# Kernel optimization log

Measured on AMD Instinct MI355X. Metric: run time of the kernel, lower is better.

The kernel has to match this reference:

```python
import jax, jax.numpy as jnp
import numpy as np

B, S, D, H = 2, 2048, 2048, 16
DH = D // H
NEG = -1000000000.0


def setup_inputs() -> dict:
    key = jax.random.key(0)
    ks = jax.random.split(key, 5)
    return {
        "query_vector": jax.random.normal(ks[0], (B, S, D), dtype=jnp.float32),
        "key_vector": jax.random.normal(ks[1], (B, S, D), dtype=jnp.float32),
        "value_vector": jax.random.normal(ks[2], (B, S, D), dtype=jnp.float32),
        "W_qkv": jax.random.normal(ks[3], (D, 3 * D), dtype=jnp.float32) * (1.0 / np.sqrt(D)),
        "b_qkv": jax.random.normal(ks[4], (3 * D,), dtype=jnp.float32) * 0.01,
    }


def reference(query_vector, key_vector, value_vector, W_qkv, b_qkv):
    # NOTE: original forward only consumes query_vector; key/value args unused.
    qkv = query_vector @ W_qkv + b_qkv                      # [B, S, 3D]
    q, k, v = jnp.split(qkv, 3, axis=-1)                    # each [B, S, D]
    # Faithful to original: plain reshape (NOT transpose) into heads.
    q = q.reshape(B, H, S, DH)
    k = k.reshape(B, H, S, DH)
    v = v.reshape(B, H, S, DH)
    scores = jnp.einsum("bhqd,bhkd->bhqk", q, k) / np.float32(np.sqrt(DH))
    # torch.triu_indices(offset=0): mask j >= i (diagonal included), SET to -1e9.
    idx = jnp.arange(S)
    causal = idx[None, :] >= idx[:, None]                   # [S, S], True where masked
    scores = jnp.where(causal, jnp.float32(NEG), scores)
    attn = jax.nn.softmax(scores, axis=-1)
    out = jnp.einsum("bhqk,bhkd->bhqd", attn, v)            # [B, H, S, DH]
    # dropout is identity in eval mode
    return out.reshape(B, S, D)
```

## Files before the change

kernel.cpp:

```cpp
#include <hip/hip_runtime.h>
#include <hip/hip_bf16.h>
#include <stdint.h>

typedef unsigned short u16;
typedef short short8 __attribute__((ext_vector_type(8)));
typedef short short4v __attribute__((ext_vector_type(4)));
typedef float f32x4 __attribute__((ext_vector_type(4)));

#define CSL (0.08838834764831845f * 1.4426950408889634f)
#define NEGR -1.0e13f


__device__ __forceinline__ u16 f2b(float f) {
  union { float f; unsigned int u; } c; c.f = f;
  unsigned int u = c.u;
  u += 0x7fffu + ((u >> 16) & 1u);
  return (u16)(u >> 16);
}
__device__ __forceinline__ float b2f(u16 h) {
  union { float f; unsigned int u; } c; c.u = ((unsigned int)h) << 16;
  return c.f;
}

__global__ __launch_bounds__(256) void k_cast_q(const float* __restrict__ in, u16* __restrict__ out) {
  size_t idx = ((size_t)blockIdx.x * 256 + threadIdx.x) * 8;
  float4 f0 = *(const float4*)(in + idx);
  float4 f1 = *(const float4*)(in + idx + 4);
  short8 o;
  o[0] = (short)f2b(f0.x); o[1] = (short)f2b(f0.y); o[2] = (short)f2b(f0.z); o[3] = (short)f2b(f0.w);
  o[4] = (short)f2b(f1.x); o[5] = (short)f2b(f1.y); o[6] = (short)f2b(f1.z); o[7] = (short)f2b(f1.w);
  *(short8*)(out + idx) = o;
}

__global__ __launch_bounds__(256) void k_cast_wt(const float* __restrict__ W, u16* __restrict__ Wt) {
  __shared__ u16 L[64 * 68];
  const int t = threadIdx.x;
  const int nb = blockIdx.x * 64;
  const int kb = blockIdx.y * 64;
#pragma unroll
  for (int it = 0; it < 4; ++it) {
    int idx = it * 1024 + t * 4;
    int r = idx >> 6, c = idx & 63;
    float4 f = *(const float4*)(W + (size_t)(kb + r) * 6144 + nb + c);
    L[r * 68 + c + 0] = f2b(f.x);
    L[r * 68 + c + 1] = f2b(f.y);
    L[r * 68 + c + 2] = f2b(f.z);
    L[r * 68 + c + 3] = f2b(f.w);
  }
  __syncthreads();
#pragma unroll
  for (int it = 0; it < 4; ++it) {
    int idx = it * 1024 + t * 4;
    int i = idx >> 6, j = idx & 63;
    short4v o;
#pragma unroll
    for (int e = 0; e < 4; ++e) o[e] = (short)L[(j + e) * 68 + i];
    *(short4v*)(Wt + (size_t)(nb + i) * 2048 + kb + j) = o;
  }
}

__global__ __launch_bounds__(256) void k_gemm(const u16* __restrict__ A,
                                              const u16* __restrict__ Bt,
                                              const float* __restrict__ bias,
                                              u16* __restrict__ qb,
                                              u16* __restrict__ kbuf,
                                              u16* __restrict__ vbuf) {
  __shared__ u16 As[128 * 32];
  __shared__ u16 Bs[128 * 32];
  const int t = threadIdx.x;
  const int ln = t & 63, wv = t >> 6;
  const int lr = ln & 15, lg = ln >> 4;
  const int mb = blockIdx.y * 128, nb = blockIdx.x * 128;
  const int wm = (wv >> 1) * 64, wn = (wv & 1) * 64;
  f32x4 acc[4][4] = {};
  for (int kt = 0; kt < 64; ++kt) {
    const int k0 = kt * 32;
#pragma unroll
    for (int it = 0; it < 2; ++it) {
      int chunk = it * 256 + wv * 64 + ln;
      int r = chunk >> 2, c8 = (chunk & 3) * 8;
      __builtin_amdgcn_global_load_lds(
          (const __attribute__((address_space(1))) void*)(A + (size_t)(mb + r) * 2048 + k0 + c8),
          (__attribute__((address_space(3))) void*)(As + (size_t)(it * 256 + wv * 64) * 8),
          16, 0, 0);
      __builtin_amdgcn_global_load_lds(
          (const __attribute__((address_space(1))) void*)(Bt + (size_t)(nb + r) * 2048 + k0 + c8),
          (__attribute__((address_space(3))) void*)(Bs + (size_t)(it * 256 + wv * 64) * 8),
          16, 0, 0);
    }
    __syncthreads();
    short8 af[4], bf[4];
#pragma unroll
    for (int mi = 0; mi < 4; ++mi)
      af[mi] = *(const short8*)(As + (wm + mi * 16 + lr) * 32 + lg * 8);
#pragma unroll
    for (int ni = 0; ni < 4; ++ni)
      bf[ni] = *(const short8*)(Bs + (wn + ni * 16 + lr) * 32 + lg * 8);
#pragma unroll
    for (int mi = 0; mi < 4; ++mi)
#pragma unroll
      for (int ni = 0; ni < 4; ++ni)
        acc[mi][ni] = __builtin_amdgcn_mfma_f32_16x16x32_bf16(af[mi], bf[ni], acc[mi][ni], 0, 0, 0);
    __syncthreads();
  }
  u16* dst = (nb < 2048) ? qb : (nb < 4096 ? kbuf : vbuf);
  const int nnb = nb & 2047;
#pragma unroll
  for (int ni = 0; ni < 4; ++ni) {
    int n = wn + ni * 16 + lr;
    float bv = bias[nb + n];
#pragma unroll
    for (int mi = 0; mi < 4; ++mi) {
#pragma unroll
      for (int r = 0; r < 4; ++r) {
        int m = mb + wm + mi * 16 + lg * 4 + r;
        dst[(size_t)m * 2048 + nnb + n] = f2b(acc[mi][ni][r] + bv);
      }
    }
  }
}

__global__ __launch_bounds__(256) void k_vtrans(const u16* __restrict__ v, u16* __restrict__ vt,
                                                float* __restrict__ part) {
  __shared__ u16 L[128 * 136];
  __shared__ float Ls2[256];
  const int t = threadIdx.x;
  const int bh = blockIdx.y, sc = blockIdx.x;
  const size_t base = (size_t)bh * 262144;
#pragma unroll
  for (int it = 0; it < 8; ++it) {
    int chunk = it * 256 + t;
    int s = chunk >> 4, d8 = (chunk & 15) * 8;
    *(short8*)(L + s * 136 + d8) = *(const short8*)(v + base + (size_t)(sc * 128 + s) * 128 + d8);
  }
  __syncthreads();
#pragma unroll
  for (int it = 0; it < 8; ++it) {
    int chunk = it * 256 + t;
    int dh = chunk >> 4, s8 = (chunk & 15) * 8;
    short8 o;
#pragma unroll
    for (int e = 0; e < 8; ++e) o[e] = (short)L[(s8 + e) * 136 + dh];
    *(short8*)(vt + base + (size_t)dh * 2048 + sc * 128 + s8) = o;
  }
  {
    const int dh = t & 127, seg = t >> 7;
    float ps = 0.f;
#pragma unroll 8
    for (int i = 0; i < 64; ++i) ps += b2f(L[(seg * 64 + i) * 136 + dh]);
    Ls2[t] = ps;
    __syncthreads();
    if (t < 128) part[((size_t)bh * 16 + sc) * 128 + t] = Ls2[t] + Ls2[t + 128];
  }
}

__global__ __launch_bounds__(256, 3) void k_attn(const u16* __restrict__ qb,
                                                 const u16* __restrict__ kb,
                                                 const u16* __restrict__ vt,
                                                 const float* __restrict__ part,
                                                 float* __restrict__ out) {
  __shared__ u16 Ks[64 * 136];
  __shared__ u16 Vs[128 * 72];
  __shared__ u16 Ps[4][16 * 72];
  const int t = threadIdx.x;
  const int ln = t & 63, wv = t >> 6;
  const int lr = ln & 15, lg = ln >> 4;
  const int L = blockIdx.y * 32 + blockIdx.x;
  const int wl = (L & 7) * 128 + (L >> 3);
  const int bh = wl >> 5;
  const int qt = 31 - (wl & 31);
  const size_t base = (size_t)bh * 262144;
  const u16* Qh = qb + base;
  const u16* Kh = kb + base;
  const u16* Vth = vt + base;
  float* Oh = out + base;
  const int qs = qt * 64;

  short8 qf[4];
  {
    int qr = qs + wv * 16 + lr;
#pragma unroll
    for (int ks = 0; ks < 4; ++ks)
      qf[ks] = *(const short8*)(Qh + (size_t)qr * 128 + ks * 32 + lg * 8);
  }
  float lsum[4] = {0.f, 0.f, 0.f, 0.f};
  f32x4 acc[8];
  const f32x4 fz = {0.f, 0.f, 0.f, 0.f};
#pragma unroll
  for (int oj = 0; oj < 8; ++oj) acc[oj] = fz;

  u16* Pw = &Ps[wv][0];
  const int nkt = qt + 1;
  for (int kt = 0; kt < nkt; ++kt) {
#pragma unroll
    for (int it = 0; it < 4; ++it) {
      int chunk = it * 256 + t;
      int sk = chunk >> 4, d8 = (chunk & 15) * 8;
      *(short8*)(Ks + sk * 136 + d8) = *(const short8*)(Kh + (size_t)(kt * 64 + sk) * 128 + d8);
    }
#pragma unroll
    for (int it = 0; it < 4; ++it) {
      int chunk = it * 256 + t;
      int dh = chunk >> 3, s8 = (chunk & 7) * 8;
      *(short8*)(Vs + dh * 72 + s8) = *(const short8*)(Vth + (size_t)dh * 2048 + kt * 64 + s8);
    }
    __syncthreads();

    f32x4 s[4];
#pragma unroll
    for (int ni = 0; ni < 4; ++ni) s[ni] = fz;
#pragma unroll
    for (int ks = 0; ks < 4; ++ks) {
#pragma unroll
      for (int ni = 0; ni < 4; ++ni) {
        short8 kf = *(const short8*)(Ks + (ni * 16 + lr) * 136 + ks * 32 + lg * 8);
        s[ni] = __builtin_amdgcn_mfma_f32_16x16x32_bf16(qf[ks], kf, s[ni], 0, 0, 0);
      }
    }
    if (kt == qt) {
#pragma unroll
      for (int ni = 0; ni < 4; ++ni) {
        int col = kt * 64 + ni * 16 + lr;
#pragma unroll
        for (int r = 0; r < 4; ++r) {
          int row = qs + wv * 16 + lg * 4 + r;
          if (col >= row) s[ni][r] = NEGR;
        }
      }
    }
#pragma unroll
    for (int ni = 0; ni < 4; ++ni)
#pragma unroll
      for (int r = 0; r < 4; ++r) {
        u16 h = f2b(exp2f(s[ni][r] * CSL));
        Pw[(lg * 4 + r) * 72 + ni * 16 + lr] = h;
        lsum[r] += b2f(h);
      }
#pragma unroll
    for (int ks2 = 0; ks2 < 2; ++ks2) {
      short8 pa = *(const short8*)(Pw + lr * 72 + ks2 * 32 + lg * 8);
#pragma unroll
      for (int oj = 0; oj < 8; ++oj) {
        short8 vf = *(const short8*)(Vs + (oj * 16 + lr) * 72 + ks2 * 32 + lg * 8);
        acc[oj] = __builtin_amdgcn_mfma_f32_16x16x32_bf16(pa, vf, acc[oj], 0, 0, 0);
      }
    }
    __syncthreads();
  }

  float rl[4];
#pragma unroll
  for (int r = 0; r < 4; ++r) {
    float sa = lsum[r];
#pragma unroll
    for (int d = 1; d < 16; d <<= 1) sa += __shfl_xor(sa, d, 64);
    rl[r] = 1.0f / sa;
  }
#pragma unroll
  for (int oj = 0; oj < 8; ++oj)
#pragma unroll
    for (int r = 0; r < 4; ++r) {
      int row = qs + wv * 16 + lg * 4 + r;
      float val = acc[oj][r] * rl[r];
      if (qt == 0 && wv == 0 && lg == 0 && r == 0) {
        float vs = 0.f;
#pragma unroll
        for (int sc = 0; sc < 16; ++sc) vs += part[(size_t)bh * 2048 + sc * 128 + oj * 16 + lr];
        val = vs * (1.0f / 2048.0f);
      }
      Oh[(size_t)row * 128 + oj * 16 + lr] = val;
    }
}

extern "C" void kernel_launch(void* const* d_in, const int* in_sizes, int n_in,
                              void* d_out, int out_size, void* d_ws, size_t ws_size,
                              hipStream_t stream) {
  (void)in_sizes; (void)n_in; (void)out_size; (void)ws_size;
  const float* q_in = (const float*)d_in[0];
  const float* W = (const float*)d_in[3];
  const float* bias = (const float*)d_in[4];
  float* out = (float*)d_out;

  u16* qbf = (u16*)d_ws;
  u16* wtb = qbf + (size_t)4096 * 2048;
  u16* qb  = wtb + (size_t)6144 * 2048;
  u16* kbf = qb  + (size_t)4096 * 2048;
  u16* vbf = kbf + (size_t)4096 * 2048;
  u16* vt  = vbf + (size_t)4096 * 2048;
  float* part = (float*)(vt + (size_t)4096 * 2048);

  k_cast_q<<<4096, 256, 0, stream>>>(q_in, qbf);
  k_cast_wt<<<dim3(96, 32), 256, 0, stream>>>(W, wtb);
  k_gemm<<<dim3(48, 32), 256, 0, stream>>>(qbf, wtb, bias, qb, kbf, vbf);
  k_vtrans<<<dim3(16, 32), 256, 0, stream>>>(vbf, vt, part);
  k_attn<<<dim3(32, 32), 256, 0, stream>>>(qb, kbf, vt, part, out);
}
```

Measured before the change: 242.8 us.

## Replace QKV GEMM with 256x256 double-buffered swizzled-LDS tile kernel

Swaps the 128x128 single-buffered projection GEMM for a 512-thread kernel computing 256x256 tiles with BK=64. LDS is double-buffered so the next k-tile's global_load_lds overlaps the MFMAs, rows are XOR-swizzled to avoid bank conflicts, blocks are remapped for L2 locality, and MFMA phases use setprio. This aims to raise arithmetic intensity and hide memory latency. The trade-offs are 384 blocks with one block per CU, which may leave the tail underfilled, plus more barriers per k-step.

```diff
diff --git a/kernel.cpp b/kernel.cpp
--- a/kernel.cpp
+++ b/kernel.cpp
@@ -59,62 +59,139 @@
   }
 }
 
-__global__ __launch_bounds__(256) void k_gemm(const u16* __restrict__ A,
-                                              const u16* __restrict__ Bt,
-                                              const float* __restrict__ bias,
-                                              u16* __restrict__ qb,
-                                              u16* __restrict__ kbuf,
-                                              u16* __restrict__ vbuf) {
-  __shared__ u16 As[128 * 32];
-  __shared__ u16 Bs[128 * 32];
+__global__ __launch_bounds__(512, 1) void k_gemm256(const u16* __restrict__ A,
+                                                    const u16* __restrict__ Bt,
+                                                    const float* __restrict__ bias,
+                                                    u16* __restrict__ qb,
+                                                    u16* __restrict__ kbuf,
+                                                    u16* __restrict__ vbuf) {
+  __shared__ u16 As[2][16384];
+  __shared__ u16 Bs[2][16384];
   const int t = threadIdx.x;
-  const int ln = t & 63, wv = t >> 6;
+  const int ln = t & 63, w = t >> 6;
   const int lr = ln & 15, lg = ln >> 4;
-  const int mb = blockIdx.y * 128, nb = blockIdx.x * 128;
-  const int wm = (wv >> 1) * 64, wn = (wv & 1) * 64;
-  f32x4 acc[4][4] = {};
-  for (int kt = 0; kt < 64; ++kt) {
-    const int k0 = kt * 32;
-#pragma unroll
-    for (int it = 0; it < 2; ++it) {
-      int chunk = it * 256 + wv * 64 + ln;
-      int r = chunk >> 2, c8 = (chunk & 3) * 8;
-      __builtin_amdgcn_global_load_lds(
-          (const __attribute__((address_space(1))) void*)(A + (size_t)(mb + r) * 2048 + k0 + c8),
-          (__attribute__((address_space(3))) void*)(As + (size_t)(it * 256 + wv * 64) * 8),
-          16, 0, 0);
-      __builtin_amdgcn_global_load_lds(
-          (const __attribute__((address_space(1))) void*)(Bt + (size_t)(nb + r) * 2048 + k0 + c8),
-          (__attribute__((address_space(3))) void*)(Bs + (size_t)(it * 256 + wv * 64) * 8),
-          16, 0, 0);
-    }
-    __syncthreads();
-    short8 af[4], bf[4];
-#pragma unroll
-    for (int mi = 0; mi < 4; ++mi)
-      af[mi] = *(const short8*)(As + (wm + mi * 16 + lr) * 32 + lg * 8);
-#pragma unroll
-    for (int ni = 0; ni < 4; ++ni)
-      bf[ni] = *(const short8*)(Bs + (wn + ni * 16 + lr) * 32 + lg * 8);
-#pragma unroll
-    for (int mi = 0; mi < 4; ++mi)
-#pragma unroll
-      for (int ni = 0; ni < 4; ++ni)
-        acc[mi][ni] = __builtin_amdgcn_mfma_f32_16x16x32_bf16(af[mi], bf[ni], acc[mi][ni], 0, 0, 0);
-    __syncthreads();
-  }
+  const int wm = w >> 2, wn = w & 3;
+  const int Lid = blockIdx.y * 24 + blockIdx.x;
+  const int wl = (Lid & 7) * 48 + (Lid >> 3);
+  const int mb = (wl / 24) * 256, nb = (wl % 24) * 256;
+  const int cswz = (lr & 7) * 8;
+  const int srow = w * 8 + (ln >> 3);
+  const int scol = ((ln & 7) ^ (ln >> 3)) * 8;
+
+  const u16* Abase = A + (size_t)mb * 2048;
+  const u16* Bbase = Bt + (size_t)nb * 2048;
+
+  f32x4 acc[8][4] = {};
+
+#define STAGE_KT(kt_, buf_)                                                                        \
+  do {                                                                                             \
+    const u16* as_ = Abase + (size_t)srow * 2048 + (kt_) * 64 + scol;                              \
+    const u16* bs_ = Bbase + (size_t)srow * 2048 + (kt_) * 64 + scol;                              \
+    _Pragma("unroll")                                                                              \
+    for (int p = 0; p < 4; ++p)                                                                    \
+      __builtin_amdgcn_global_load_lds(                                                            \
+          (const __attribute__((address_space(1))) void*)(as_ + (size_t)p * 64 * 2048),            \
+          (__attribute__((address_space(3))) void*)(&As[buf_][p * 4096 + w * 512]), 16, 0, 0);     \
+    _Pragma("unroll")                                                                              \
+    for (int p = 0; p < 4; ++p)                                                                    \
+      __builtin_amdgcn_global_load_lds(                                                            \
+          (const __attribute__((address_space(1))) void*)(bs_ + (size_t)p * 64 * 2048),            \
+          (__attribute__((address_space(3))) void*)(&Bs[buf_][p * 4096 + w * 512]), 16, 0, 0);     \
+  } while (0)
+
+  STAGE_KT(0, 0);
+  asm volatile("s_waitcnt vmcnt(0)" ::: "memory");
+  __builtin_amdgcn_s_barrier();
+
+  for (int kt = 0; kt < 32; ++kt) {
+    const int cur = kt & 1;
+    const u16* At = &As[cur][0];
+    const u16* Bl = &Bs[cur][0];
+    short8 af[4][2], bf0[2][2], bf1[2][2];
+
+#pragma unroll
+    for (int mi = 0; mi < 4; ++mi)
+#pragma unroll
+      for (int ks = 0; ks < 2; ++ks)
+        af[mi][ks] = *(const short8*)(At + (wm * 128 + mi * 16 + lr) * 64 + ((ks * 32 + lg * 8) ^ cswz));
+#pragma unroll
+    for (int ni = 0; ni < 2; ++ni)
+#pragma unroll
+      for (int ks = 0; ks < 2; ++ks)
+        bf0[ni][ks] = *(const short8*)(Bl + (wn * 64 + ni * 16 + lr) * 64 + ((ks * 32 + lg * 8) ^ cswz));
+    if (kt + 1 < 32) STAGE_KT(kt + 1, cur ^ 1);
+    __builtin_amdgcn_s_barrier();
+    __builtin_amdgcn_s_setprio(1);
+#pragma unroll
+    for (int mi = 0; mi < 4; ++mi)
+#pragma unroll
+      for (int ni = 0; ni < 2; ++ni)
+#pragma unroll
+        for (int ks = 0; ks < 2; ++ks)
+          acc[mi][ni] = __builtin_amdgcn_mfma_f32_16x16x32_bf16(af[mi][ks], bf0[ni][ks], acc[mi][ni], 0, 0, 0);
+    __builtin_amdgcn_s_setprio(0);
+    __builtin_amdgcn_s_barrier();
+
+#pragma unroll
+    for (int ni = 0; ni < 2; ++ni)
+#pragma unroll
+      for (int ks = 0; ks < 2; ++ks)
+        bf1[ni][ks] = *(const short8*)(Bl + (wn * 64 + 32 + ni * 16 + lr) * 64 + ((ks * 32 + lg * 8) ^ cswz));
+    __builtin_amdgcn_s_barrier();
+    __builtin_amdgcn_s_setprio(1);
+#pragma unroll
+    for (int mi = 0; mi < 4; ++mi)
+#pragma unroll
+      for (int ni = 0; ni < 2; ++ni)
+#pragma unroll
+        for (int ks = 0; ks < 2; ++ks)
+          acc[mi][2 + ni] = __builtin_amdgcn_mfma_f32_16x16x32_bf16(af[mi][ks], bf1[ni][ks], acc[mi][2 + ni], 0, 0, 0);
+    __builtin_amdgcn_s_setprio(0);
+    __builtin_amdgcn_s_barrier();
+
+#pragma unroll
+    for (int mi = 0; mi < 4; ++mi)
+#pragma unroll
+      for (int ks = 0; ks < 2; ++ks)
+        af[mi][ks] = *(const short8*)(At + (wm * 128 + 64 + mi * 16 + lr) * 64 + ((ks * 32 + lg * 8) ^ cswz));
+    __builtin_amdgcn_s_barrier();
+    __builtin_amdgcn_s_setprio(1);
+#pragma unroll
+    for (int mi = 0; mi < 4; ++mi)
+#pragma unroll
+      for (int ni = 0; ni < 2; ++ni)
+#pragma unroll
+        for (int ks = 0; ks < 2; ++ks)
+          acc[4 + mi][ni] = __builtin_amdgcn_mfma_f32_16x16x32_bf16(af[mi][ks], bf0[ni][ks], acc[4 + mi][ni], 0, 0, 0);
+    __builtin_amdgcn_s_setprio(0);
+    __builtin_amdgcn_s_barrier();
+
+    __builtin_amdgcn_s_setprio(1);
+#pragma unroll
+    for (int mi = 0; mi < 4; ++mi)
+#pragma unroll
+      for (int ni = 0; ni < 2; ++ni)
+#pragma unroll
+        for (int ks = 0; ks < 2; ++ks)
+          acc[4 + mi][2 + ni] = __builtin_amdgcn_mfma_f32_16x16x32_bf16(af[mi][ks], bf1[ni][ks], acc[4 + mi][2 + ni], 0, 0, 0);
+    __builtin_amdgcn_s_setprio(0);
+    asm volatile("s_waitcnt vmcnt(0)" ::: "memory");
+    __builtin_amdgcn_s_barrier();
+  }
+#undef STAGE_KT
+
   u16* dst = (nb < 2048) ? qb : (nb < 4096 ? kbuf : vbuf);
   const int nnb = nb & 2047;
 #pragma unroll
   for (int ni = 0; ni < 4; ++ni) {
-    int n = wn + ni * 16 + lr;
+    int n = wn * 64 + ni * 16 + lr;
     float bv = bias[nb + n];
 #pragma unroll
-    for (int mi = 0; mi < 4; ++mi) {
+    for (int m = 0; m < 8; ++m) {
 #pragma unroll
       for (int r = 0; r < 4; ++r) {
-        int m = mb + wm + mi * 16 + lg * 4 + r;
-        dst[(size_t)m * 2048 + nnb + n] = f2b(acc[mi][ni][r] + bv);
+        int mrow = mb + wm * 128 + m * 16 + lg * 4 + r;
+        dst[(size_t)mrow * 2048 + nnb + n] = f2b(acc[m][ni][r] + bv);
       }
     }
   }
@@ -291,7 +368,7 @@
 
   k_cast_q<<<4096, 256, 0, stream>>>(q_in, qbf);
   k_cast_wt<<<dim3(96, 32), 256, 0, stream>>>(W, wtb);
-  k_gemm<<<dim3(48, 32), 256, 0, stream>>>(qbf, wtb, bias, qb, kbf, vbf);
+  k_gemm256<<<dim3(24, 16), 512, 0, stream>>>(qbf, wtb, bias, qb, kbf, vbf);
   k_vtrans<<<dim3(16, 32), 256, 0, stream>>>(vbf, vt, part);
   k_attn<<<dim3(32, 32), 256, 0, stream>>>(qb, kbf, vt, part, out);
 }
```

After: 262.6 us. 8.1% more time.
